# Kernel tuning notes

Hardware: AMD Instinct MI355X
Metric: run time of the kernel (lower is better)

The kernel has to match this reference:

```python
import jax, jax.numpy as jnp
import numpy as np

N_NODES = 50000
N_EDGES = 600000
N_RELS = 19
D_IN = 128
D_HID = 64
D_OUT = 2


def setup_inputs() -> dict:
    key = jax.random.key(0)
    ks = jax.random.split(key, 10)
    feat = jax.random.normal(ks[0], (N_NODES, D_IN), dtype=jnp.float32)
    src = jax.random.randint(ks[1], (N_EDGES,), 0, N_NODES)
    dst = jax.random.randint(ks[2], (N_EDGES,), 0, N_NODES)
    etype = jax.random.randint(ks[3], (N_EDGES,), 0, N_RELS)
    s1 = 1.0 / np.sqrt(D_IN)
    s2 = 1.0 / np.sqrt(D_HID)
    W1 = jax.random.normal(ks[4], (N_RELS, D_IN, D_HID), dtype=jnp.float32) * s1
    loop1 = jax.random.normal(ks[5], (D_IN, D_HID), dtype=jnp.float32) * s1
    b1 = jnp.zeros((D_HID,), dtype=jnp.float32)
    W2 = jax.random.normal(ks[6], (N_RELS, D_HID, D_OUT), dtype=jnp.float32) * s2
    loop2 = jax.random.normal(ks[7], (D_HID, D_OUT), dtype=jnp.float32) * s2
    b2 = jnp.zeros((D_OUT,), dtype=jnp.float32)
    return {"feat": feat, "W1": W1, "loop1": loop1, "b1": b1,
            "W2": W2, "loop2": loop2, "b2": b2,
            "src": src, "dst": dst, "etype": etype}


def _rel_graph_conv(h, W, loop_w, bias, src, dst, etype, activation):
    # Per-relation transform of all nodes: [N, R, O]; then gather per edge.
    # (num_rels * out_feat is small, so this is cheaper than gathering W per edge.)
    transformed = jnp.einsum('nd,rdo->nro', h, W)
    msg = transformed[src, etype]                      # [E, O] edge messages
    agg = jax.ops.segment_sum(msg, dst, num_segments=h.shape[0])  # scatter-add
    out = agg + h @ loop_w + bias                      # self-loop + bias
    if activation is not None:
        out = activation(out)
    return out


def reference(feat, W1, loop1, b1, W2, loop2, b2, src, dst, etype):
    h = _rel_graph_conv(feat, W1, loop1, b1, src, dst, etype, jax.nn.relu)
    h = _rel_graph_conv(h, W2, loop2, b2, src, dst, etype, None)
    return h
```

## Files before the change

### kernel.cpp

```cpp
#include <hip/hip_runtime.h>

#define N_NODES 50000
#define N_EDGES 600000
#define N_RELS  19
#define D_IN    128
#define D_HID   64
#define D_OUT   2
#define BSH     9
#define NB      ((N_NODES + 511) >> 9)
#define NSEG    (NB * N_RELS)
#define SL_BLOCKS  ((N_NODES + 63) / 64)
#define PREP_ELEMS (N_RELS * D_HID * D_IN + 48 * 64 + D_HID * D_IN)
#define PREP_BLOCKS ((PREP_ELEMS + 255) / 256)

typedef unsigned short u16;
typedef unsigned int   u32;
typedef __attribute__((ext_vector_type(8))) short sfrag;
typedef __attribute__((ext_vector_type(4))) float f32x4;

__device__ __forceinline__ u16 f2bf(float f){
  union { float f; u32 i; } v; v.f = f;
  u32 r = v.i + 0x7fffu + ((v.i >> 16) & 1u);
  return (u16)(r >> 16);
}
__device__ __forceinline__ float bf2f(u16 u){
  union { u32 i; float f; } v; v.i = ((u32)u) << 16; return v.f;
}
__device__ __forceinline__ u32 pack2(float lo, float hi){
  return (u32)f2bf(lo) | ((u32)f2bf(hi) << 16);
}

__global__ __launch_bounds__(256) void k_fused_pre(const float* __restrict__ feat,
                                                   u16* __restrict__ featb,
                                                   const int* __restrict__ src,
                                                   const int* __restrict__ et,
                                                   const int* __restrict__ dst,
                                                   int* __restrict__ seg_hist,
                                                   int* __restrict__ hist_dst){
  int i = blockIdx.x * 256 + threadIdx.x;
  float4 f = ((const float4*)feat)[i];
  uint2 p; p.x = pack2(f.x, f.y); p.y = pack2(f.z, f.w);
  ((uint2*)featb)[i] = p;
  if (i < N_EDGES) {
    int key = (src[i] >> BSH) * N_RELS + et[i];
    atomicAdd(&seg_hist[key * 16], 1);
    atomicAdd(&hist_dst[dst[i]], 1);
  }
}

__global__ __launch_bounds__(256) void k_alloc_scan(
    const int* __restrict__ hist_dst, int* __restrict__ dstart,
    int* __restrict__ cur_dst, int* __restrict__ gcnt,
    const int* __restrict__ seg_hist, int* __restrict__ seg_off,
    int* __restrict__ cur_seg,
    const float* __restrict__ W1, const float* __restrict__ loop1,
    const float* __restrict__ W2, u16* __restrict__ W1Tb,
    u16* __restrict__ loop1Tb, u16* __restrict__ W2allT){
  if (blockIdx.x >= 197) {
    int idx = (blockIdx.x - 197) * 256 + threadIdx.x;
    const int T1 = N_RELS * D_HID * D_IN;
    const int T2c = T1 + 48 * 64;
    const int T3 = T2c + D_HID * D_IN;
    if (idx < T1) {
      int r = idx / (D_HID * D_IN);
      int t = idx - r * (D_HID * D_IN);
      int j = t >> 7, d = t & 127;
      W1Tb[idx] = f2bf(W1[(r * D_IN + d) * D_HID + j]);
    } else if (idx < T2c) {
      int k2 = idx - T1;
      int n = k2 >> 6, k = k2 & 63;
      float val = 0.f;
      if (n < N_RELS * D_OUT) {
        int r = n >> 1, o = n & 1;
        val = W2[(r * D_HID + k) * D_OUT + o];
      }
      W2allT[k2] = f2bf(val);
    } else if (idx < T3) {
      int k2 = idx - T2c;
      int j = k2 >> 7, d = k2 & 127;
      loop1Tb[k2] = f2bf(loop1[d * D_HID + j]);
    }
    return;
  }
  if (blockIdx.x == 196) {
    __shared__ int se_s[256];
    int tid = threadIdx.x;
    const int PER = (NSEG + 255) / 256;
    int lo = tid * PER, hi = lo + PER; if (hi > NSEG) hi = NSEG; if (lo > NSEG) lo = NSEG;
    int se = 0;
    for (int i = lo; i < hi; ++i) se += seg_hist[i * 16];
    se_s[tid] = se;
    __syncthreads();
    if (tid == 0) {
      int a = 0;
      for (int j = 0; j < 256; ++j) { int x = se_s[j]; se_s[j] = a; a += x; }
    }
    __syncthreads();
    int eo = se_s[tid];
    for (int i = lo; i < hi; ++i) {
      int c = seg_hist[i * 16];
      seg_off[i] = eo; cur_seg[i * 16] = eo;
      eo += c;
    }
    if (hi == NSEG) seg_off[NSEG] = eo;
    return;
  }
  __shared__ int wbase[4];
  int tid = threadIdx.x, lane = tid & 63, wv = tid >> 6;
  int n = blockIdx.x * 256 + tid;
  int v = (n < N_NODES) ? hist_dst[n] : 0;
  int x = v;
  #pragma unroll
  for (int o = 1; o < 64; o <<= 1) { int u = __shfl_up(x, o); if (lane >= o) x += u; }
  if (lane == 63) wbase[wv] = atomicAdd(gcnt, x);
  __syncthreads();
  int start = wbase[wv] + x - v;
  if (n < N_NODES) { dstart[n] = start; cur_dst[n] = start; }
}

__global__ __launch_bounds__(256) void k_scatter(const int* __restrict__ src,
                                                 const int* __restrict__ et,
                                                 int* __restrict__ cur_seg,
                                                 int* __restrict__ perm){
  int e = blockIdx.x * 256 + threadIdx.x;
  if (e >= N_EDGES) return;
  int key = (src[e] >> BSH) * N_RELS + et[e];
  int p = atomicAdd(&cur_seg[key * 16], 1);
  perm[p] = e;
}

__device__ __forceinline__ void gather_tile(
    const u16* __restrict__ featb, const int* __restrict__ src,
    const int* __restrict__ dst, const int* __restrict__ perm,
    int* __restrict__ cur_dst, int* __restrict__ srel,
    int ts, int c, int t0, int rel, int tid, int w, int r16, int c4,
    sfrag (&aN)[2][4], int& nextPos){
  int vc = c - t0; if (vc > 128) vc = 128;
  #pragma unroll
  for (int mt = 0; mt < 2; ++mt) {
    int row = w * 32 + mt * 16 + r16;
    int rr = row < vc ? row : vc - 1;
    int s = src[perm[ts + t0 + rr]];
    const u16* ap = featb + (size_t)s * D_IN + c4 * 8;
    #pragma unroll
    for (int kk = 0; kk < 4; ++kk)
      aN[mt][kk] = *(const sfrag*)(ap + kk * 32);
  }
  nextPos = -1;
  if (tid < 128 && tid < vc) {
    int e = perm[ts + t0 + tid];
    nextPos = atomicAdd(&cur_dst[dst[e]], 1);
    srel[nextPos] = (src[e] << 5) | rel;
  }
}

__global__ __launch_bounds__(256, 4) void k_se1(
    const u16* __restrict__ featb, const u16* __restrict__ W1Tb,
    const u16* __restrict__ loop1Tb, const float* __restrict__ b1,
    const int* __restrict__ src, const int* __restrict__ dst,
    const int* __restrict__ perm, const int* __restrict__ seg_off,
    int* __restrict__ cur_dst, int* __restrict__ srel,
    u16* __restrict__ msgbuf, u16* __restrict__ agg1b){
  __shared__ __align__(16) u16 Bls[64][136];
  __shared__ __align__(16) u16 msg[128][72];
  __shared__ int posIds[128];
  int tid = threadIdx.x, lane = tid & 63, w = tid >> 6;
  int r16 = lane & 15, c4 = lane >> 4;

  if (blockIdx.x >= NSEG) {
    int base = (blockIdx.x - NSEG) * 64;
    { int j = tid >> 2, sg = tid & 3;
      const uint4* g = (const uint4*)(loop1Tb + j * 128) + sg * 4;
      uint4* d = (uint4*)&Bls[j][sg * 32];
      d[0] = g[0]; d[1] = g[1]; d[2] = g[2]; d[3] = g[3]; }
    int arow = base + w * 16 + r16; if (arow >= N_NODES) arow = N_NODES - 1;
    sfrag aF[4];
    #pragma unroll
    for (int kk = 0; kk < 4; ++kk)
      aF[kk] = *(const sfrag*)(featb + (size_t)arow * D_IN + kk * 32 + c4 * 8);
    __syncthreads();
    #pragma unroll
    for (int ct = 0; ct < 4; ++ct) {
      f32x4 acc = {0.f, 0.f, 0.f, 0.f};
      #pragma unroll
      for (int kk = 0; kk < 4; ++kk) {
        sfrag bF = *(const sfrag*)&Bls[ct * 16 + r16][kk * 32 + c4 * 8];
        acc = __builtin_amdgcn_mfma_f32_16x16x32_bf16(aF[kk], bF, acc, 0, 0, 0);
      }
      int col = ct * 16 + r16;
      float bias = b1[col];
      #pragma unroll
      for (int reg = 0; reg < 4; ++reg) {
        float v = acc[reg] + bias;
        float o = __shfl_xor(v, 1);
        if (!(lane & 1)) {
          int orow = w * 16 + c4 * 4 + reg;
          *(u32*)&msg[orow][col] = pack2(v, o);
        }
      }
    }
    __syncthreads();
    { int row = tid >> 2, q = tid & 3;
      int n = base + row;
      if (n < N_NODES) {
        uint4 a0 = ((const uint4*)&msg[row][0])[q * 2];
        uint4 a1 = ((const uint4*)&msg[row][0])[q * 2 + 1];
        uint4* d = (uint4*)(agg1b + (size_t)n * D_HID + q * 16);
        d[0] = a0; d[1] = a1;
      } }
    return;
  }

  const int q8 = NSEG >> 3, r8 = NSEG & 7;
  int xcd = blockIdx.x & 7, cidx = blockIdx.x >> 3;
  int seg = (xcd < r8 ? xcd * (q8 + 1) : r8 * (q8 + 1) + (xcd - r8) * q8) + cidx;
  int ts = seg_off[seg], c = seg_off[seg + 1] - ts;
  if (c == 0) return;
  int rel = seg - (seg / N_RELS) * N_RELS;

  {
    int j = tid >> 2, sg = tid & 3;
    const uint4* g = (const uint4*)(W1Tb + ((size_t)rel * 64 + j) * 128) + sg * 4;
    uint4* d = (uint4*)&Bls[j][sg * 32];
    d[0] = g[0]; d[1] = g[1]; d[2] = g[2]; d[3] = g[3];
  }

  sfrag aN[2][4]; int nextPos;
  gather_tile(featb, src, dst, perm, cur_dst, srel, ts, c, 0, rel,
              tid, w, r16, c4, aN, nextPos);
  __syncthreads();

  for (int t0 = 0; t0 < c; t0 += 128) {
    sfrag aC[2][4];
    #pragma unroll
    for (int mt = 0; mt < 2; ++mt)
      #pragma unroll
      for (int kk = 0; kk < 4; ++kk) aC[mt][kk] = aN[mt][kk];
    int curPos = nextPos;
    if (t0 + 128 < c)
      gather_tile(featb, src, dst, perm, cur_dst, srel, ts, c, t0 + 128, rel,
                  tid, w, r16, c4, aN, nextPos);
    #pragma unroll
    for (int ct = 0; ct < 4; ++ct) {
      sfrag bF[4];
      #pragma unroll
      for (int kk = 0; kk < 4; ++kk)
        bF[kk] = *(const sfrag*)&Bls[ct * 16 + r16][kk * 32 + c4 * 8];
      #pragma unroll
      for (int mt = 0; mt < 2; ++mt) {
        f32x4 acc = {0.f, 0.f, 0.f, 0.f};
        #pragma unroll
        for (int kk = 0; kk < 4; ++kk)
          acc = __builtin_amdgcn_mfma_f32_16x16x32_bf16(aC[mt][kk], bF[kk], acc, 0, 0, 0);
        #pragma unroll
        for (int reg = 0; reg < 4; ++reg) {
          float v = acc[reg];
          float o = __shfl_xor(v, 1);
          if (!(lane & 1)) {
            int orow = w * 32 + mt * 16 + c4 * 4 + reg;
            *(u32*)&msg[orow][ct * 16 + r16] = pack2(v, o);
          }
        }
      }
    }
    if (tid < 128) posIds[tid] = curPos;
    __syncthreads();
    { int row = tid >> 1, half = tid & 1;
      int pos = posIds[row];
      if (pos >= 0) {
        const uint4* mr = (const uint4*)&msg[row][half * 32];
        uint4* d = (uint4*)(msgbuf + (size_t)pos * D_HID + half * 32);
        d[0] = mr[0]; d[1] = mr[1]; d[2] = mr[2]; d[3] = mr[3];
      } }
    __syncthreads();
  }
}

__global__ __launch_bounds__(256) void k_agg_relu_self2(
    const u16* __restrict__ msgbuf, const int* __restrict__ dstart,
    const int* __restrict__ cnt, const u16* __restrict__ agg1b,
    const float* __restrict__ loop2, const float* __restrict__ b2,
    u16* __restrict__ h1b, float* __restrict__ out){
  int wv = threadIdx.x >> 6, lane = threadIdx.x & 63;
  int n = blockIdx.x * 4 + wv;
  int s = dstart[n], epos = s + cnt[n];
  int h = lane >> 5, c = lane & 31;
  float a0 = 0.f, a1 = 0.f;
  for (int i = s + h; i < epos; i += 2) {
    u32 v = ((const u32*)msgbuf)[(size_t)i * 32 + c];
    a0 += bf2f((u16)(v & 0xffffu));
    a1 += bf2f((u16)(v >> 16));
  }
  a0 += __shfl_down(a0, 32);
  a1 += __shfl_down(a1, 32);
  float p0 = 0.f, p1 = 0.f;
  if (h == 0) {
    u32 sv = ((const u32*)agg1b)[(size_t)n * 32 + c];
    float v0 = a0 + bf2f((u16)(sv & 0xffffu));
    float v1 = a1 + bf2f((u16)(sv >> 16));
    v0 = v0 > 0.f ? v0 : 0.f;
    v1 = v1 > 0.f ? v1 : 0.f;
    ((u32*)h1b)[(size_t)n * 32 + c] = (u32)f2bf(v0) | ((u32)f2bf(v1) << 16);
    float2 w0 = ((const float2*)loop2)[2 * c];
    float2 w1 = ((const float2*)loop2)[2 * c + 1];
    p0 = v0 * w0.x + v1 * w1.x;
    p1 = v0 * w0.y + v1 * w1.y;
  }
  #pragma unroll
  for (int off = 16; off; off >>= 1) {
    p0 += __shfl_down(p0, off);
    p1 += __shfl_down(p1, off);
  }
  if (lane == 0) {
    out[n * 2]     = p0 + b2[0];
    out[n * 2 + 1] = p1 + b2[1];
  }
}

__global__ __launch_bounds__(256) void k_t2(
    const u16* __restrict__ h1b, const u16* __restrict__ W2allT,
    float* __restrict__ T2){
  __shared__ __align__(16) u16 Bls[48][72];
  int tid = threadIdx.x, lane = tid & 63, w = tid >> 6;
  int r16 = lane & 15, c4 = lane >> 4;
  for (int idx = tid; idx < 48 * 8; idx += 256) {
    int row = idx >> 3, q = idx & 7;
    ((uint4*)&Bls[row][0])[q] = ((const uint4*)W2allT)[idx];
  }
  int base = blockIdx.x * 64;
  int arow = base + w * 16 + r16; if (arow >= N_NODES) arow = N_NODES - 1;
  sfrag aF[2];
  #pragma unroll
  for (int kk = 0; kk < 2; ++kk)
    aF[kk] = *(const sfrag*)(h1b + (size_t)arow * D_HID + kk * 32 + c4 * 8);
  __syncthreads();
  #pragma unroll
  for (int ct = 0; ct < 3; ++ct) {
    f32x4 acc = {0.f, 0.f, 0.f, 0.f};
    #pragma unroll
    for (int kk = 0; kk < 2; ++kk) {
      sfrag bF = *(const sfrag*)&Bls[ct * 16 + r16][kk * 32 + c4 * 8];
      acc = __builtin_amdgcn_mfma_f32_16x16x32_bf16(aF[kk], bF, acc, 0, 0, 0);
    }
    int col = ct * 16 + r16;
    if (col < N_RELS * D_OUT) {
      #pragma unroll
      for (int reg = 0; reg < 4; ++reg) {
        int orow = base + w * 16 + c4 * 4 + reg;
        if (orow < N_NODES) T2[(size_t)orow * 40 + col] = acc[reg];
      }
    }
  }
}

__global__ __launch_bounds__(256) void k_fin(
    const float* __restrict__ T2, const int* __restrict__ srel,
    const int* __restrict__ dstart, const int* __restrict__ cnt,
    float* __restrict__ out){
  int wv = threadIdx.x >> 6, lane = threadIdx.x & 63;
  int n = blockIdx.x * 4 + wv;
  int s = dstart[n], c = cnt[n];
  float ax = 0.f, ay = 0.f;
  for (int i = lane; i < c; i += 64) {
    int sr = srel[s + i];
    const float* p = T2 + (size_t)(sr >> 5) * 40 + (sr & 31) * 2;
    ax += p[0]; ay += p[1];
  }
  #pragma unroll
  for (int off = 32; off; off >>= 1) {
    ax += __shfl_down(ax, off);
    ay += __shfl_down(ay, off);
  }
  if (lane == 0) {
    out[n * 2]     += ax;
    out[n * 2 + 1] += ay;
  }
}

extern "C" void kernel_launch(void* const* d_in, const int* in_sizes, int n_in,
                              void* d_out, int out_size, void* d_ws, size_t ws_size,
                              hipStream_t stream){
  const float* feat  = (const float*)d_in[0];
  const float* W1    = (const float*)d_in[1];
  const float* loop1 = (const float*)d_in[2];
  const float* b1    = (const float*)d_in[3];
  const float* W2    = (const float*)d_in[4];
  const float* loop2 = (const float*)d_in[5];
  const float* b2    = (const float*)d_in[6];
  const int* src     = (const int*)d_in[7];
  const int* dst     = (const int*)d_in[8];
  const int* et      = (const int*)d_in[9];
  float* out = (float*)d_out;

  char* w = (char*)d_ws;
  u16*   W1Tb     = (u16*)(w);
  u16*   W2allT   = (u16*)(w + 311296);
  u16*   loop1Tb  = (u16*)(w + 317440);
  int*   seg_hist = (int*)(w + 333824);
  int*   gcnt     = (int*)(w + 452992);
  int*   hist_dst = (int*)(w + 453056);
  int*   seg_off  = (int*)(w + 653056);
  int*   cur_seg  = (int*)(w + 660544);
  int*   dstart   = (int*)(w + 779712);
  int*   cur_dst  = (int*)(w + 979712);
  int*   perm     = (int*)(w + 1179712);
  int*   srel     = (int*)(w + 3579712);
  u16*   featb    = (u16*)(w + 5979712);
  float* T2f      = (float*)(w + 5979712);
  u16*   agg1b    = (u16*)(w + 18779712);
  u16*   h1b      = (u16*)(w + 25179712);
  u16*   msgbuf   = (u16*)(w + 31579712);

  hipMemsetAsync(w + 333824, 0, 319232, stream);
  k_fused_pre     <<<6250, 256, 0, stream>>>(feat, featb, src, et, dst, seg_hist, hist_dst);
  k_alloc_scan    <<<197 + PREP_BLOCKS, 256, 0, stream>>>(
                      hist_dst, dstart, cur_dst, gcnt, seg_hist, seg_off, cur_seg,
                      W1, loop1, W2, W1Tb, loop1Tb, W2allT);
  k_scatter       <<<2344,  256, 0, stream>>>(src, et, cur_seg, perm);
  k_se1           <<<NSEG + SL_BLOCKS, 256, 0, stream>>>(
                      featb, W1Tb, loop1Tb, b1, src, dst, perm, seg_off,
                      cur_dst, srel, msgbuf, agg1b);
  k_agg_relu_self2<<<12500, 256, 0, stream>>>(msgbuf, dstart, hist_dst, agg1b,
                                              loop2, b2, h1b, out);
  k_t2            <<<SL_BLOCKS, 256, 0, stream>>>(h1b, W2allT, T2f);
  k_fin           <<<12500, 256, 0, stream>>>(T2f, srel, dstart, hist_dst, out);
}
```

Baseline: 302.4 us.

## Fuse all stages into one persistent cooperative kernel with grid syncs

Replaces the memset and seven separate kernel launches with a single cooperative persistent kernel. Each stage loops over virtual block indices and is separated from the next by grid.sync(), which removes per-launch gaps and the memset call. Layer-2 aggregation is also restructured: loop2 is folded into the transposed W2 matrix, and the ReLU, self-loop and per-relation transform are done in one pass with a scalar LDS dot product, replacing the MFMA k_t2 kernel and the h1b round trip. The cost is grid-wide barriers, a grid capped at the occupancy limit, and one register and LDS budget shared by every stage.

```diff
diff --git a/kernel.cpp b/kernel.cpp
--- a/kernel.cpp
+++ b/kernel.cpp
@@ -1,4 +1,6 @@
 #include <hip/hip_runtime.h>
+#include <hip/hip_cooperative_groups.h>
+namespace cg = cooperative_groups;
 
 #define N_NODES 50000
 #define N_EDGES 600000
@@ -9,9 +11,10 @@
 #define BSH     9
 #define NB      ((N_NODES + 511) >> 9)
 #define NSEG    (NB * N_RELS)
-#define SL_BLOCKS  ((N_NODES + 63) / 64)
-#define PREP_ELEMS (N_RELS * D_HID * D_IN + 48 * 64 + D_HID * D_IN)
-#define PREP_BLOCKS ((PREP_ELEMS + 255) / 256)
+#define SL_BLOCKS ((N_NODES + 63) / 64)
+#define PREP_ELEMS (N_RELS * D_HID * D_IN + 64 * 64 + D_HID * D_IN)
+#define ZERO_INTS (319232 / 4)
+#define NAGG 12500
 
 typedef unsigned short u16;
 typedef unsigned int   u32;
@@ -30,37 +33,66 @@
   return (u32)f2bf(lo) | ((u32)f2bf(hi) << 16);
 }
 
-__global__ __launch_bounds__(256) void k_fused_pre(const float* __restrict__ feat,
-                                                   u16* __restrict__ featb,
-                                                   const int* __restrict__ src,
-                                                   const int* __restrict__ et,
-                                                   const int* __restrict__ dst,
-                                                   int* __restrict__ seg_hist,
-                                                   int* __restrict__ hist_dst){
-  int i = blockIdx.x * 256 + threadIdx.x;
-  float4 f = ((const float4*)feat)[i];
-  uint2 p; p.x = pack2(f.x, f.y); p.y = pack2(f.z, f.w);
-  ((uint2*)featb)[i] = p;
-  if (i < N_EDGES) {
-    int key = (src[i] >> BSH) * N_RELS + et[i];
-    atomicAdd(&seg_hist[key * 16], 1);
-    atomicAdd(&hist_dst[dst[i]], 1);
-  }
-}
-
-__global__ __launch_bounds__(256) void k_alloc_scan(
-    const int* __restrict__ hist_dst, int* __restrict__ dstart,
-    int* __restrict__ cur_dst, int* __restrict__ gcnt,
-    const int* __restrict__ seg_hist, int* __restrict__ seg_off,
-    int* __restrict__ cur_seg,
-    const float* __restrict__ W1, const float* __restrict__ loop1,
-    const float* __restrict__ W2, u16* __restrict__ W1Tb,
-    u16* __restrict__ loop1Tb, u16* __restrict__ W2allT){
-  if (blockIdx.x >= 197) {
-    int idx = (blockIdx.x - 197) * 256 + threadIdx.x;
-    const int T1 = N_RELS * D_HID * D_IN;
-    const int T2c = T1 + 48 * 64;
-    const int T3 = T2c + D_HID * D_IN;
+__device__ __forceinline__ void gather_tile(
+    const u16* __restrict__ featb, const int* __restrict__ src,
+    const int* __restrict__ dst, const int* __restrict__ perm,
+    int* __restrict__ cur_dst, int* __restrict__ srel,
+    int ts, int c, int t0, int rel, int tid, int w4, int r16, int c4,
+    sfrag (&aN)[2][4], int& nextPos){
+  int vc = c - t0; if (vc > 128) vc = 128;
+  #pragma unroll
+  for (int mt = 0; mt < 2; ++mt) {
+    int row = w4 * 32 + mt * 16 + r16;
+    int rr = row < vc ? row : vc - 1;
+    int s = src[perm[ts + t0 + rr]];
+    const u16* ap = featb + (size_t)s * D_IN + c4 * 8;
+    #pragma unroll
+    for (int kk = 0; kk < 4; ++kk)
+      aN[mt][kk] = *(const sfrag*)(ap + kk * 32);
+  }
+  nextPos = -1;
+  if (tid < 128 && tid < vc) {
+    int e = perm[ts + t0 + tid];
+    nextPos = atomicAdd(&cur_dst[dst[e]], 1);
+    srel[nextPos] = (src[e] << 5) | rel;
+  }
+}
+
+__global__ __launch_bounds__(256, 4) void k_all(
+    const float* __restrict__ feat, const float* __restrict__ W1,
+    const float* __restrict__ loop1, const float* __restrict__ b1,
+    const float* __restrict__ W2, const float* __restrict__ loop2,
+    const float* __restrict__ b2, const int* __restrict__ src,
+    const int* __restrict__ dst, const int* __restrict__ et,
+    float* __restrict__ out, char* __restrict__ ws){
+  u16*   W1Tb     = (u16*)(ws);
+  u16*   W2allT   = (u16*)(ws + 311296);
+  u16*   loop1Tb  = (u16*)(ws + 319488);
+  int*   seg_hist = (int*)(ws + 335872);
+  int*   gcnt     = (int*)(ws + 455040);
+  int*   hist_dst = (int*)(ws + 455104);
+  int*   seg_off  = (int*)(ws + 655104);
+  int*   cur_seg  = (int*)(ws + 662592);
+  int*   dstart   = (int*)(ws + 781760);
+  int*   cur_dst  = (int*)(ws + 981760);
+  int*   perm     = (int*)(ws + 1181760);
+  int*   srel     = (int*)(ws + 3581760);
+  u16*   featb    = (u16*)(ws + 5981760);
+  u16*   agg1b    = (u16*)(ws + 18781760);
+  float* T2f      = (float*)(ws + 25181760);
+  u16*   msgbuf   = (u16*)(ws + 33181760);
+
+  __shared__ __align__(16) char smem[36864];
+  cg::grid_group grid = cg::this_grid();
+  const int tid = threadIdx.x, lane = tid & 63, w4 = tid >> 6;
+  const int bid = blockIdx.x, G = gridDim.x;
+  const int r16 = lane & 15, c4 = lane >> 4;
+  const int gth = G * 256;
+
+  for (int i = bid * 256 + tid; i < ZERO_INTS; i += gth) seg_hist[i] = 0;
+  for (int idx = bid * 256 + tid; idx < PREP_ELEMS; idx += gth) {
+    const int T1  = N_RELS * D_HID * D_IN;
+    const int T2c = T1 + 64 * 64;
     if (idx < T1) {
       int r = idx / (D_HID * D_IN);
       int t = idx - r * (D_HID * D_IN);
@@ -68,312 +100,238 @@
       W1Tb[idx] = f2bf(W1[(r * D_IN + d) * D_HID + j]);
     } else if (idx < T2c) {
       int k2 = idx - T1;
-      int n = k2 >> 6, k = k2 & 63;
+      int j = k2 >> 6, k = k2 & 63;
       float val = 0.f;
-      if (n < N_RELS * D_OUT) {
-        int r = n >> 1, o = n & 1;
-        val = W2[(r * D_HID + k) * D_OUT + o];
-      }
+      if (j < N_RELS * D_OUT)      val = W2[((j >> 1) * D_HID + k) * D_OUT + (j & 1)];
+      else if (j == 38)            val = loop2[k * 2];
+      else if (j == 39)            val = loop2[k * 2 + 1];
       W2allT[k2] = f2bf(val);
-    } else if (idx < T3) {
+    } else {
       int k2 = idx - T2c;
       int j = k2 >> 7, d = k2 & 127;
       loop1Tb[k2] = f2bf(loop1[d * D_HID + j]);
     }
-    return;
-  }
-  if (blockIdx.x == 196) {
-    __shared__ int se_s[256];
-    int tid = threadIdx.x;
+  }
+  grid.sync();
+
+  for (int i = bid * 256 + tid; i < N_NODES * D_IN / 4; i += gth) {
+    float4 f = ((const float4*)feat)[i];
+    uint2 p; p.x = pack2(f.x, f.y); p.y = pack2(f.z, f.w);
+    ((uint2*)featb)[i] = p;
+  }
+  for (int e = bid * 256 + tid; e < N_EDGES; e += gth) {
+    int key = (src[e] >> BSH) * N_RELS + et[e];
+    atomicAdd(&seg_hist[key * 16], 1);
+    atomicAdd(&hist_dst[dst[e]], 1);
+  }
+  grid.sync();
+
+  if (bid == 0) {
+    int* ps = (int*)smem;
     const int PER = (NSEG + 255) / 256;
     int lo = tid * PER, hi = lo + PER; if (hi > NSEG) hi = NSEG; if (lo > NSEG) lo = NSEG;
-    int se = 0;
-    for (int i = lo; i < hi; ++i) se += seg_hist[i * 16];
-    se_s[tid] = se;
+    int s = 0;
+    for (int i = lo; i < hi; ++i) s += seg_hist[i * 16];
+    ps[tid] = s;
     __syncthreads();
-    if (tid == 0) {
-      int a = 0;
-      for (int j = 0; j < 256; ++j) { int x = se_s[j]; se_s[j] = a; a += x; }
-    }
+    if (tid == 0) { int a = 0; for (int j = 0; j < 256; ++j) { int x = ps[j]; ps[j] = a; a += x; } }
     __syncthreads();
-    int eo = se_s[tid];
+    int eo = ps[tid];
     for (int i = lo; i < hi; ++i) {
-      int c = seg_hist[i * 16];
+      int cs = seg_hist[i * 16];
       seg_off[i] = eo; cur_seg[i * 16] = eo;
-      eo += c;
+      eo += cs;
     }
     if (hi == NSEG) seg_off[NSEG] = eo;
-    return;
-  }
-  __shared__ int wbase[4];
-  int tid = threadIdx.x, lane = tid & 63, wv = tid >> 6;
-  int n = blockIdx.x * 256 + tid;
-  int v = (n < N_NODES) ? hist_dst[n] : 0;
-  int x = v;
-  #pragma unroll
-  for (int o = 1; o < 64; o <<= 1) { int u = __shfl_up(x, o); if (lane >= o) x += u; }
-  if (lane == 63) wbase[wv] = atomicAdd(gcnt, x);
-  __syncthreads();
-  int start = wbase[wv] + x - v;
-  if (n < N_NODES) { dstart[n] = start; cur_dst[n] = start; }
-}
-
-__global__ __launch_bounds__(256) void k_scatter(const int* __restrict__ src,
-                                                 const int* __restrict__ et,
-                                                 int* __restrict__ cur_seg,
-                                                 int* __restrict__ perm){
-  int e = blockIdx.x * 256 + threadIdx.x;
-  if (e >= N_EDGES) return;
-  int key = (src[e] >> BSH) * N_RELS + et[e];
-  int p = atomicAdd(&cur_seg[key * 16], 1);
-  perm[p] = e;
-}
-
-__device__ __forceinline__ void gather_tile(
-    const u16* __restrict__ featb, const int* __restrict__ src,
-    const int* __restrict__ dst, const int* __restrict__ perm,
-    int* __restrict__ cur_dst, int* __restrict__ srel,
-    int ts, int c, int t0, int rel, int tid, int w, int r16, int c4,
-    sfrag (&aN)[2][4], int& nextPos){
-  int vc = c - t0; if (vc > 128) vc = 128;
-  #pragma unroll
-  for (int mt = 0; mt < 2; ++mt) {
-    int row = w * 32 + mt * 16 + r16;
-    int rr = row < vc ? row : vc - 1;
-    int s = src[perm[ts + t0 + rr]];
-    const u16* ap = featb + (size_t)s * D_IN + c4 * 8;
+  } else if (bid <= 196) {
+    int* wbase = (int*)smem;
+    int n = (bid - 1) * 256 + tid;
+    int vv = (n < N_NODES) ? hist_dst[n] : 0;
+    int x = vv;
     #pragma unroll
-    for (int kk = 0; kk < 4; ++kk)
-      aN[mt][kk] = *(const sfrag*)(ap + kk * 32);
-  }
-  nextPos = -1;
-  if (tid < 128 && tid < vc) {
-    int e = perm[ts + t0 + tid];
-    nextPos = atomicAdd(&cur_dst[dst[e]], 1);
-    srel[nextPos] = (src[e] << 5) | rel;
-  }
-}
-
-__global__ __launch_bounds__(256, 4) void k_se1(
-    const u16* __restrict__ featb, const u16* __restrict__ W1Tb,
-    const u16* __restrict__ loop1Tb, const float* __restrict__ b1,
-    const int* __restrict__ src, const int* __restrict__ dst,
-    const int* __restrict__ perm, const int* __restrict__ seg_off,
-    int* __restrict__ cur_dst, int* __restrict__ srel,
-    u16* __restrict__ msgbuf, u16* __restrict__ agg1b){
-  __shared__ __align__(16) u16 Bls[64][136];
-  __shared__ __align__(16) u16 msg[128][72];
-  __shared__ int posIds[128];
-  int tid = threadIdx.x, lane = tid & 63, w = tid >> 6;
-  int r16 = lane & 15, c4 = lane >> 4;
-
-  if (blockIdx.x >= NSEG) {
-    int base = (blockIdx.x - NSEG) * 64;
-    { int j = tid >> 2, sg = tid & 3;
-      const uint4* g = (const uint4*)(loop1Tb + j * 128) + sg * 4;
-      uint4* d = (uint4*)&Bls[j][sg * 32];
-      d[0] = g[0]; d[1] = g[1]; d[2] = g[2]; d[3] = g[3]; }
-    int arow = base + w * 16 + r16; if (arow >= N_NODES) arow = N_NODES - 1;
-    sfrag aF[4];
-    #pragma unroll
-    for (int kk = 0; kk < 4; ++kk)
-      aF[kk] = *(const sfrag*)(featb + (size_t)arow * D_IN + kk * 32 + c4 * 8);
+    for (int o = 1; o < 64; o <<= 1) { int u = __shfl_up(x, o); if (lane >= o) x += u; }
+    if (lane == 63) wbase[w4] = atomicAdd(gcnt, x);
     __syncthreads();
-    #pragma unroll
-    for (int ct = 0; ct < 4; ++ct) {
-      f32x4 acc = {0.f, 0.f, 0.f, 0.f};
-      #pragma unroll
-      for (int kk = 0; kk < 4; ++kk) {
-        sfrag bF = *(const sfrag*)&Bls[ct * 16 + r16][kk * 32 + c4 * 8];
-        acc = __builtin_amdgcn_mfma_f32_16x16x32_bf16(aF[kk], bF, acc, 0, 0, 0);
-      }
-      int col = ct * 16 + r16;
-      float bias = b1[col];
-      #pragma unroll
-      for (int reg = 0; reg < 4; ++reg) {
-        float v = acc[reg] + bias;
-        float o = __shfl_xor(v, 1);
-        if (!(lane & 1)) {
-          int orow = w * 16 + c4 * 4 + reg;
-          *(u32*)&msg[orow][col] = pack2(v, o);
+    int start = wbase[w4] + x - vv;
+    if (n < N_NODES) { dstart[n] = start; cur_dst[n] = start; }
+  }
+  grid.sync();
+
+  for (int e = bid * 256 + tid; e < N_EDGES; e += gth) {
+    int key = (src[e] >> BSH) * N_RELS + et[e];
+    int p = atomicAdd(&cur_seg[key * 16], 1);
+    perm[p] = e;
+  }
+  grid.sync();
+
+  {
+    u16 (*Bls)[136] = (u16(*)[136])smem;
+    u16 (*msgl)[72] = (u16(*)[72])(smem + 17408);
+    int* posIds     = (int*)(smem + 35840);
+    for (int v = bid; v < NSEG + SL_BLOCKS; v += G) {
+      if (v >= NSEG) {
+        int base = (v - NSEG) * 64;
+        { int j = tid >> 2, sg = tid & 3;
+          const uint4* g = (const uint4*)(loop1Tb + j * 128) + sg * 4;
+          uint4* d = (uint4*)&Bls[j][sg * 32];
+          d[0] = g[0]; d[1] = g[1]; d[2] = g[2]; d[3] = g[3]; }
+        int arow = base + w4 * 16 + r16; if (arow >= N_NODES) arow = N_NODES - 1;
+        sfrag aF[4];
+        #pragma unroll
+        for (int kk = 0; kk < 4; ++kk)
+          aF[kk] = *(const sfrag*)(featb + (size_t)arow * D_IN + kk * 32 + c4 * 8);
+        __syncthreads();
+        #pragma unroll
+        for (int ct = 0; ct < 4; ++ct) {
+          f32x4 acc = {0.f, 0.f, 0.f, 0.f};
+          #pragma unroll
+          for (int kk = 0; kk < 4; ++kk) {
+            sfrag bF = *(const sfrag*)&Bls[ct * 16 + r16][kk * 32 + c4 * 8];
+            acc = __builtin_amdgcn_mfma_f32_16x16x32_bf16(aF[kk], bF, acc, 0, 0, 0);
+          }
+          int col = ct * 16 + r16;
+          float bias = b1[col];
+          #pragma unroll
+          for (int reg = 0; reg < 4; ++reg) {
+            float vv2 = acc[reg] + bias;
+            float o = __shfl_xor(vv2, 1);
+            if (!(lane & 1)) {
+              int orow = w4 * 16 + c4 * 4 + reg;
+              *(u32*)&msgl[orow][col] = pack2(vv2, o);
+            }
+          }
+        }
+        __syncthreads();
+        { int row = tid >> 2, q = tid & 3;
+          int n = base + row;
+          if (n < N_NODES) {
+            uint4 a0 = ((const uint4*)&msgl[row][0])[q * 2];
+            uint4 a1 = ((const uint4*)&msgl[row][0])[q * 2 + 1];
+            uint4* d = (uint4*)(agg1b + (size_t)n * D_HID + q * 16);
+            d[0] = a0; d[1] = a1;
+          } }
+      } else {
+        const int q8 = NSEG >> 3, r8 = NSEG & 7;
+        int xcd = v & 7, cidx = v >> 3;
+        int seg = (xcd < r8 ? xcd * (q8 + 1) : r8 * (q8 + 1) + (xcd - r8) * q8) + cidx;
+        int ts = seg_off[seg], c = seg_off[seg + 1] - ts;
+        if (c == 0) continue;
+        int rel = seg - (seg / N_RELS) * N_RELS;
+        { int j = tid >> 2, sg = tid & 3;
+          const uint4* g = (const uint4*)(W1Tb + ((size_t)rel * 64 + j) * 128) + sg * 4;
+          uint4* d = (uint4*)&Bls[j][sg * 32];
+          d[0] = g[0]; d[1] = g[1]; d[2] = g[2]; d[3] = g[3]; }
+        sfrag aN[2][4]; int nextPos;
+        gather_tile(featb, src, dst, perm, cur_dst, srel, ts, c, 0, rel,
+                    tid, w4, r16, c4, aN, nextPos);
+        __syncthreads();
+        for (int t0 = 0; t0 < c; t0 += 128) {
+          sfrag aC[2][4];
+          #pragma unroll
+          for (int mt = 0; mt < 2; ++mt)
+            #pragma unroll
+            for (int kk = 0; kk < 4; ++kk) aC[mt][kk] = aN[mt][kk];
+          int curPos = nextPos;
+          if (t0 + 128 < c)
+            gather_tile(featb, src, dst, perm, cur_dst, srel, ts, c, t0 + 128, rel,
+                        tid, w4, r16, c4, aN, nextPos);
+          #pragma unroll
+          for (int ct = 0; ct < 4; ++ct) {
+            sfrag bF[4];
+            #pragma unroll
+            for (int kk = 0; kk < 4; ++kk)
+              bF[kk] = *(const sfrag*)&Bls[ct * 16 + r16][kk * 32 + c4 * 8];
+            #pragma unroll
+            for (int mt = 0; mt < 2; ++mt) {
+              f32x4 acc = {0.f, 0.f, 0.f, 0.f};
+              #pragma unroll
+              for (int kk = 0; kk < 4; ++kk)
+                acc = __builtin_amdgcn_mfma_f32_16x16x32_bf16(aC[mt][kk], bF[kk], acc, 0, 0, 0);
+              #pragma unroll
+              for (int reg = 0; reg < 4; ++reg) {
+                float vv2 = acc[reg];
+                float o = __shfl_xor(vv2, 1);
+                if (!(lane & 1)) {
+                  int orow = w4 * 32 + mt * 16 + c4 * 4 + reg;
+                  *(u32*)&msgl[orow][ct * 16 + r16] = pack2(vv2, o);
+                }
+              }
+            }
+          }
+          if (tid < 128) posIds[tid] = curPos;
+          __syncthreads();
+          { int row = tid >> 1, half = tid & 1;
+            int pos = posIds[row];
+            if (pos >= 0) {
+              const uint4* mr = (const uint4*)&msgl[row][half * 32];
+              uint4* d = (uint4*)(msgbuf + (size_t)pos * D_HID + half * 32);
+              d[0] = mr[0]; d[1] = mr[1]; d[2] = mr[2]; d[3] = mr[3];
+            } }
+          __syncthreads();
         }
       }
-    }
+      __syncthreads();
+    }
+  }
+  grid.sync();
+
+  {
+    u16   (*W2ls)[66] = (u16(*)[66])smem;
+    float (*h1s)[68]  = (float(*)[68])(smem + 8448);
+    for (int i = tid; i < 64 * 64; i += 256) W2ls[i >> 6][i & 63] = W2allT[i];
     __syncthreads();
-    { int row = tid >> 2, q = tid & 3;
-      int n = base + row;
-      if (n < N_NODES) {
-        uint4 a0 = ((const uint4*)&msg[row][0])[q * 2];
-        uint4 a1 = ((const uint4*)&msg[row][0])[q * 2 + 1];
-        uint4* d = (uint4*)(agg1b + (size_t)n * D_HID + q * 16);
-        d[0] = a0; d[1] = a1;
-      } }
-    return;
-  }
-
-  const int q8 = NSEG >> 3, r8 = NSEG & 7;
-  int xcd = blockIdx.x & 7, cidx = blockIdx.x >> 3;
-  int seg = (xcd < r8 ? xcd * (q8 + 1) : r8 * (q8 + 1) + (xcd - r8) * q8) + cidx;
-  int ts = seg_off[seg], c = seg_off[seg + 1] - ts;
-  if (c == 0) return;
-  int rel = seg - (seg / N_RELS) * N_RELS;
-
-  {
-    int j = tid >> 2, sg = tid & 3;
-    const uint4* g = (const uint4*)(W1Tb + ((size_t)rel * 64 + j) * 128) + sg * 4;
-    uint4* d = (uint4*)&Bls[j][sg * 32];
-    d[0] = g[0]; d[1] = g[1]; d[2] = g[2]; d[3] = g[3];
-  }
-
-  sfrag aN[2][4]; int nextPos;
-  gather_tile(featb, src, dst, perm, cur_dst, srel, ts, c, 0, rel,
-              tid, w, r16, c4, aN, nextPos);
-  __syncthreads();
-
-  for (int t0 = 0; t0 < c; t0 += 128) {
-    sfrag aC[2][4];
+    int h = lane >> 5, cc = lane & 31;
+    for (int v = bid; v < NAGG; v += G) {
+      int n = v * 4 + w4;
+      int s = dstart[n], epos = s + hist_dst[n];
+      float a0 = 0.f, a1 = 0.f;
+      for (int i = s + h; i < epos; i += 2) {
+        u32 mv = ((const u32*)msgbuf)[(size_t)i * 32 + cc];
+        a0 += bf2f((u16)(mv & 0xffffu));
+        a1 += bf2f((u16)(mv >> 16));
+      }
+      a0 += __shfl_down(a0, 32);
+      a1 += __shfl_down(a1, 32);
+      if (h == 0) {
+        u32 sv = ((const u32*)agg1b)[(size_t)n * 32 + cc];
+        float v0 = a0 + bf2f((u16)(sv & 0xffffu));
+        float v1 = a1 + bf2f((u16)(sv >> 16));
+        v0 = v0 > 0.f ? v0 : 0.f;
+        v1 = v1 > 0.f ? v1 : 0.f;
+        h1s[w4][2 * cc] = v0;
+        h1s[w4][2 * cc + 1] = v1;
+      }
+      int j = lane;
+      if (j < 40) {
+        float acc = 0.f;
+        #pragma unroll 8
+        for (int k = 0; k < 64; ++k)
+          acc += bf2f(W2ls[j][k]) * h1s[w4][k];
+        if (j < 38) T2f[(size_t)n * 40 + j] = acc;
+        else        out[n * 2 + (j - 38)] = acc + b2[j - 38];
+      }
+    }
+  }
+  grid.sync();
+
+  for (int v = bid; v < NAGG; v += G) {
+    int n = v * 4 + w4;
+    int s = dstart[n], c = hist_dst[n];
+    float ax = 0.f, ay = 0.f;
+    for (int i = lane; i < c; i += 64) {
+      int sr = srel[s + i];
+      const float* p = T2f + (size_t)(sr >> 5) * 40 + (sr & 31) * 2;
+      ax += p[0]; ay += p[1];
+    }
     #pragma unroll
-    for (int mt = 0; mt < 2; ++mt)
-      #pragma unroll
-      for (int kk = 0; kk < 4; ++kk) aC[mt][kk] = aN[mt][kk];
-    int curPos = nextPos;
-    if (t0 + 128 < c)
-      gather_tile(featb, src, dst, perm, cur_dst, srel, ts, c, t0 + 128, rel,
-                  tid, w, r16, c4, aN, nextPos);
-    #pragma unroll
-    for (int ct = 0; ct < 4; ++ct) {
-      sfrag bF[4];
-      #pragma unroll
-      for (int kk = 0; kk < 4; ++kk)
-        bF[kk] = *(const sfrag*)&Bls[ct * 16 + r16][kk * 32 + c4 * 8];
-      #pragma unroll
-      for (int mt = 0; mt < 2; ++mt) {
-        f32x4 acc = {0.f, 0.f, 0.f, 0.f};
-        #pragma unroll
-        for (int kk = 0; kk < 4; ++kk)
-          acc = __builtin_amdgcn_mfma_f32_16x16x32_bf16(aC[mt][kk], bF[kk], acc, 0, 0, 0);
-        #pragma unroll
-        for (int reg = 0; reg < 4; ++reg) {
-          float v = acc[reg];
-          float o = __shfl_xor(v, 1);
-          if (!(lane & 1)) {
-            int orow = w * 32 + mt * 16 + c4 * 4 + reg;
-            *(u32*)&msg[orow][ct * 16 + r16] = pack2(v, o);
-          }
-        }
-      }
-    }
-    if (tid < 128) posIds[tid] = curPos;
-    __syncthreads();
-    { int row = tid >> 1, half = tid & 1;
-      int pos = posIds[row];
-      if (pos >= 0) {
-        const uint4* mr = (const uint4*)&msg[row][half * 32];
-        uint4* d = (uint4*)(msgbuf + (size_t)pos * D_HID + half * 32);
-        d[0] = mr[0]; d[1] = mr[1]; d[2] = mr[2]; d[3] = mr[3];
-      } }
-    __syncthreads();
-  }
-}
-
-__global__ __launch_bounds__(256) void k_agg_relu_self2(
-    const u16* __restrict__ msgbuf, const int* __restrict__ dstart,
-    const int* __restrict__ cnt, const u16* __restrict__ agg1b,
-    const float* __restrict__ loop2, const float* __restrict__ b2,
-    u16* __restrict__ h1b, float* __restrict__ out){
-  int wv = threadIdx.x >> 6, lane = threadIdx.x & 63;
-  int n = blockIdx.x * 4 + wv;
-  int s = dstart[n], epos = s + cnt[n];
-  int h = lane >> 5, c = lane & 31;
-  float a0 = 0.f, a1 = 0.f;
-  for (int i = s + h; i < epos; i += 2) {
-    u32 v = ((const u32*)msgbuf)[(size_t)i * 32 + c];
-    a0 += bf2f((u16)(v & 0xffffu));
-    a1 += bf2f((u16)(v >> 16));
-  }
-  a0 += __shfl_down(a0, 32);
-  a1 += __shfl_down(a1, 32);
-  float p0 = 0.f, p1 = 0.f;
-  if (h == 0) {
-    u32 sv = ((const u32*)agg1b)[(size_t)n * 32 + c];
-    float v0 = a0 + bf2f((u16)(sv & 0xffffu));
-    float v1 = a1 + bf2f((u16)(sv >> 16));
-    v0 = v0 > 0.f ? v0 : 0.f;
-    v1 = v1 > 0.f ? v1 : 0.f;
-    ((u32*)h1b)[(size_t)n * 32 + c] = (u32)f2bf(v0) | ((u32)f2bf(v1) << 16);
-    float2 w0 = ((const float2*)loop2)[2 * c];
-    float2 w1 = ((const float2*)loop2)[2 * c + 1];
-    p0 = v0 * w0.x + v1 * w1.x;
-    p1 = v0 * w0.y + v1 * w1.y;
-  }
-  #pragma unroll
-  for (int off = 16; off; off >>= 1) {
-    p0 += __shfl_down(p0, off);
-    p1 += __shfl_down(p1, off);
-  }
-  if (lane == 0) {
-    out[n * 2]     = p0 + b2[0];
-    out[n * 2 + 1] = p1 + b2[1];
-  }
-}
-
-__global__ __launch_bounds__(256) void k_t2(
-    const u16* __restrict__ h1b, const u16* __restrict__ W2allT,
-    float* __restrict__ T2){
-  __shared__ __align__(16) u16 Bls[48][72];
-  int tid = threadIdx.x, lane = tid & 63, w = tid >> 6;
-  int r16 = lane & 15, c4 = lane >> 4;
-  for (int idx = tid; idx < 48 * 8; idx += 256) {
-    int row = idx >> 3, q = idx & 7;
-    ((uint4*)&Bls[row][0])[q] = ((const uint4*)W2allT)[idx];
-  }
-  int base = blockIdx.x * 64;
-  int arow = base + w * 16 + r16; if (arow >= N_NODES) arow = N_NODES - 1;
-  sfrag aF[2];
-  #pragma unroll
-  for (int kk = 0; kk < 2; ++kk)
-    aF[kk] = *(const sfrag*)(h1b + (size_t)arow * D_HID + kk * 32 + c4 * 8);
-  __syncthreads();
-  #pragma unroll
-  for (int ct = 0; ct < 3; ++ct) {
-    f32x4 acc = {0.f, 0.f, 0.f, 0.f};
-    #pragma unroll
-    for (int kk = 0; kk < 2; ++kk) {
-      sfrag bF = *(const sfrag*)&Bls[ct * 16 + r16][kk * 32 + c4 * 8];
-      acc = __builtin_amdgcn_mfma_f32_16x16x32_bf16(aF[kk], bF, acc, 0, 0, 0);
-    }
-    int col = ct * 16 + r16;
-    if (col < N_RELS * D_OUT) {
-      #pragma unroll
-      for (int reg = 0; reg < 4; ++reg) {
-        int orow = base + w * 16 + c4 * 4 + reg;
-        if (orow < N_NODES) T2[(size_t)orow * 40 + col] = acc[reg];
-      }
-    }
-  }
-}
-
-__global__ __launch_bounds__(256) void k_fin(
-    const float* __restrict__ T2, const int* __restrict__ srel,
-    const int* __restrict__ dstart, const int* __restrict__ cnt,
-    float* __restrict__ out){
-  int wv = threadIdx.x >> 6, lane = threadIdx.x & 63;
-  int n = blockIdx.x * 4 + wv;
-  int s = dstart[n], c = cnt[n];
-  float ax = 0.f, ay = 0.f;
-  for (int i = lane; i < c; i += 64) {
-    int sr = srel[s + i];
-    const float* p = T2 + (size_t)(sr >> 5) * 40 + (sr & 31) * 2;
-    ax += p[0]; ay += p[1];
-  }
-  #pragma unroll
-  for (int off = 32; off; off >>= 1) {
-    ax += __shfl_down(ax, off);
-    ay += __shfl_down(ay, off);
-  }
-  if (lane == 0) {
-    out[n * 2]     += ax;
-    out[n * 2 + 1] += ay;
+    for (int off = 32; off; off >>= 1) {
+      ax += __shfl_down(ax, off);
+      ay += __shfl_down(ay, off);
+    }
+    if (lane == 0) {
+      out[n * 2]     += ax;
+      out[n * 2 + 1] += ay;
+    }
   }
 }
 
@@ -391,37 +349,25 @@
   const int* dst     = (const int*)d_in[8];
   const int* et      = (const int*)d_in[9];
   float* out = (float*)d_out;
-
-  char* w = (char*)d_ws;
-  u16*   W1Tb     = (u16*)(w);
-  u16*   W2allT   = (u16*)(w + 311296);
-  u16*   loop1Tb  = (u16*)(w + 317440);
-  int*   seg_hist = (int*)(w + 333824);
-  int*   gcnt     = (int*)(w + 452992);
-  int*   hist_dst = (int*)(w + 453056);
-  int*   seg_off  = (int*)(w + 653056);
-  int*   cur_seg  = (int*)(w + 660544);
-  int*   dstart   = (int*)(w + 779712);
-  int*   cur_dst  = (int*)(w + 979712);
-  int*   perm     = (int*)(w + 1179712);
-  int*   srel     = (int*)(w + 3579712);
-  u16*   featb    = (u16*)(w + 5979712);
-  float* T2f      = (float*)(w + 5979712);
-  u16*   agg1b    = (u16*)(w + 18779712);
-  u16*   h1b      = (u16*)(w + 25179712);
-  u16*   msgbuf   = (u16*)(w + 31579712);
-
-  hipMemsetAsync(w + 333824, 0, 319232, stream);
-  k_fused_pre     <<<6250, 256, 0, stream>>>(feat, featb, src, et, dst, seg_hist, hist_dst);
-  k_alloc_scan    <<<197 + PREP_BLOCKS, 256, 0, stream>>>(
-                      hist_dst, dstart, cur_dst, gcnt, seg_hist, seg_off, cur_seg,
-                      W1, loop1, W2, W1Tb, loop1Tb, W2allT);
-  k_scatter       <<<2344,  256, 0, stream>>>(src, et, cur_seg, perm);
-  k_se1           <<<NSEG + SL_BLOCKS, 256, 0, stream>>>(
-                      featb, W1Tb, loop1Tb, b1, src, dst, perm, seg_off,
-                      cur_dst, srel, msgbuf, agg1b);
-  k_agg_relu_self2<<<12500, 256, 0, stream>>>(msgbuf, dstart, hist_dst, agg1b,
-                                              loop2, b2, h1b, out);
-  k_t2            <<<SL_BLOCKS, 256, 0, stream>>>(h1b, W2allT, T2f);
-  k_fin           <<<12500, 256, 0, stream>>>(T2f, srel, dstart, hist_dst, out);
-}
+  char* wsb = (char*)d_ws;
+
+  static int s_grid = 0;
+  if (s_grid == 0) {
+    int nb = 0, ncu = 0;
+    hipOccupancyMaxActiveBlocksPerMultiprocessor(&nb, reinterpret_cast<const void*>(k_all), 256, 0);
+    hipDeviceGetAttribute(&ncu, hipDeviceAttributeMultiprocessorCount, 0);
+    if (nb < 1) nb = 1;
+    if (ncu < 1) ncu = 256;
+    long g = (long)nb * (long)ncu;
+    if (g > 2048) g = 2048;
+    g &= ~7L;
+    if (g < 8) g = 8;
+    s_grid = (int)g;
+  }
+
+  void* kargs[] = { (void*)&feat, (void*)&W1, (void*)&loop1, (void*)&b1,
+                    (void*)&W2, (void*)&loop2, (void*)&b2, (void*)&src,
+                    (void*)&dst, (void*)&et, (void*)&out, (void*)&wsb };
+  hipLaunchCooperativeKernel(reinterpret_cast<void*>(k_all),
+                             dim3(s_grid), dim3(256), kargs, 0, stream);
+}
```

Measured after the change: 767.6 us. 2.54x slower.
